# Optimization experiments

Measured on AMD Instinct MI355X. Metric: run time of the kernel, lower is better.

Reference implementation:

```python
import jax, jax.numpy as jnp
import numpy as np

DIM = 512
HEADS = 8


def setup_inputs() -> dict:
    key = jax.random.key(0)
    ks = jax.random.split(key, 9)
    s = 1.0 / np.sqrt(DIM)
    x = jax.random.normal(ks[0], (2, 4096, DIM), dtype=jnp.float32)
    Wq = jax.random.uniform(ks[1], (DIM, DIM), jnp.float32, -s, s)
    bq = jax.random.uniform(ks[2], (DIM,), jnp.float32, -s, s)
    Wk = jax.random.uniform(ks[3], (DIM, DIM), jnp.float32, -s, s)
    bk = jax.random.uniform(ks[4], (DIM,), jnp.float32, -s, s)
    Wv = jax.random.uniform(ks[5], (DIM, DIM), jnp.float32, -s, s)
    bv = jax.random.uniform(ks[6], (DIM,), jnp.float32, -s, s)
    Wo = jax.random.uniform(ks[7], (DIM, DIM), jnp.float32, -s, s)
    bo = jax.random.uniform(ks[8], (DIM,), jnp.float32, -s, s)
    return {"x": x, "Wq": Wq, "bq": bq, "Wk": Wk, "bk": bk,
            "Wv": Wv, "bv": bv, "Wo": Wo, "bo": bo}


def reference(x, Wq, bq, Wk, bk, Wv, bv, Wo, bo):
    b, t, d = x.shape
    h = HEADS
    dq = d // h
    scale = dq ** -0.5
    # projections: torch Linear is x @ W.T + b
    q = (x @ Wq.T + bq).reshape(b, t, h, dq)
    k = (x @ Wk.T + bk).reshape(b, t, h, dq)
    v = (x @ Wv.T + bv).reshape(b, t, h, dq)
    # attention scores [b, h, t, t] (full O(T^2) matrix, as in the original)
    att = jnp.einsum("bqhd,bkhd->bhqk", q, k) * scale
    att = jax.nn.softmax(att, axis=-1)
    out = jnp.einsum("bhqk,bkhd->bqhd", att, v).reshape(b, t, d)
    return out @ Wo.T + bo
```

## Files before the change

kernel.cpp:

```cpp
#include <hip/hip_runtime.h>

typedef short bf16x8 __attribute__((ext_vector_type(8)));
typedef float f32x4 __attribute__((ext_vector_type(4)));
typedef unsigned u32x2 __attribute__((ext_vector_type(2)));
typedef unsigned u32x4 __attribute__((ext_vector_type(4)));

#define MFMA(a, b, c) __builtin_amdgcn_mfma_f32_16x16x32_bf16((a), (b), (c), 0, 0, 0)

__device__ __forceinline__ unsigned cvtpk(float a, float b) {
    unsigned r;
    asm("v_cvt_pk_bf16_f32 %0, %1, %2" : "=v"(r) : "v"(a), "v"(b));
    return r;
}

__device__ __forceinline__ void gload16(const void* g, void* l) {
    __builtin_amdgcn_global_load_lds(
        (const __attribute__((address_space(1))) unsigned*)g,
        (__attribute__((address_space(3))) unsigned*)l, 16, 0, 0);
}

__global__ __launch_bounds__(256) void cvt_kernel(
    const float* __restrict__ x,
    const float* __restrict__ w0, const float* __restrict__ w1,
    const float* __restrict__ w2, const float* __restrict__ w3,
    unsigned short* __restrict__ xd,
    unsigned short* __restrict__ d0, unsigned short* __restrict__ d1,
    unsigned short* __restrict__ d2, unsigned short* __restrict__ d3)
{
    int bid = blockIdx.x;
    const float* src;
    unsigned short* dst;
    int off;
    if (bid < 4096) { src = x; dst = xd; off = bid; }
    else {
        int s = (bid - 4096) >> 8;
        src = s == 0 ? w0 : (s == 1 ? w1 : (s == 2 ? w2 : w3));
        dst = s == 0 ? d0 : (s == 1 ? d1 : (s == 2 ? d2 : d3));
        off = (bid - 4096) & 255;
    }
    size_t i = ((size_t)off * 256 + threadIdx.x) * 4;
    float4 v = *(const float4*)(src + i);
    uint2 pk;
    pk.x = cvtpk(v.x, v.y);
    pk.y = cvtpk(v.z, v.w);
    *(uint2*)(dst + i) = pk;
}

__device__ __forceinline__ void gemm128_core(
    const unsigned short* __restrict__ A, const unsigned short* __restrict__ W,
    int m0, int n0, int tid, unsigned short* sA, unsigned short* sB,
    f32x4 acc[4][4])
{
    const int lane = tid & 63, wid = tid >> 6;
    const int quad = lane >> 4, l15 = lane & 15;
    const int wm = wid >> 1, wn = wid & 1;

    const int gl_r = lane >> 3;
    const int gl_kc = (lane & 7) ^ gl_r;

    #pragma unroll
    for (int i = 0; i < 4; i++)
        #pragma unroll
        for (int j = 0; j < 4; j++) {
            f32x4 z = {0.f, 0.f, 0.f, 0.f};
            acc[i][j] = z;
        }

    for (int k0 = 0; k0 < 512; k0 += 64) {
        #pragma unroll
        for (int p = 0; p < 4; p++) {
            int chunk = wid * 4 + p;
            int row = chunk * 8 + gl_r;
            gload16(A + (size_t)(m0 + row) * 512 + k0 + gl_kc * 8,
                    (char*)sA + chunk * 1024);
            gload16(W + (size_t)(n0 + row) * 512 + k0 + gl_kc * 8,
                    (char*)sB + chunk * 1024);
        }
        __syncthreads();
        #pragma unroll
        for (int ks = 0; ks < 2; ks++) {
            bf16x8 af[4], bfr[4];
            #pragma unroll
            for (int i = 0; i < 4; i++) {
                int row = wm * 64 + i * 16 + l15;
                int kc = ks * 4 + quad;
                af[i] = *(const bf16x8*)((const char*)sA + row * 128 + ((kc ^ (row & 7)) << 4));
            }
            #pragma unroll
            for (int j = 0; j < 4; j++) {
                int row = wn * 64 + j * 16 + l15;
                int kc = ks * 4 + quad;
                bfr[j] = *(const bf16x8*)((const char*)sB + row * 128 + ((kc ^ (row & 7)) << 4));
            }
            #pragma unroll
            for (int i = 0; i < 4; i++)
                #pragma unroll
                for (int j = 0; j < 4; j++)
                    acc[i][j] = MFMA(af[i], bfr[j], acc[i][j]);
        }
        __syncthreads();
    }
}

__global__ __launch_bounds__(256) void qkv_kernel(
    const unsigned short* __restrict__ x,
    const unsigned short* __restrict__ Wq, const float* __restrict__ bq,
    const unsigned short* __restrict__ Wk, const float* __restrict__ bk,
    const unsigned short* __restrict__ Wv, const float* __restrict__ bv,
    unsigned short* __restrict__ qo, unsigned short* __restrict__ ko,
    unsigned short* __restrict__ vo)
{
    __shared__ unsigned short sA[128 * 64];
    __shared__ unsigned short sB[128 * 64];
    const int tid = threadIdx.x;
    const int by = blockIdx.y;
    const int sel = by >> 2;
    const int n0 = (by & 3) * 128;
    const int m0 = blockIdx.x * 128;
    const unsigned short* W = sel == 0 ? Wq : (sel == 1 ? Wk : Wv);
    const float* bias = sel == 0 ? bq : (sel == 1 ? bk : bv);

    f32x4 acc[4][4];
    gemm128_core(x, W, m0, n0, tid, sA, sB, acc);

    const int lane = tid & 63, wid = tid >> 6;
    const int quad = lane >> 4, l15 = lane & 15;
    const int wm = wid >> 1, wn = wid & 1;
    float bv4[4];
    #pragma unroll
    for (int j = 0; j < 4; j++) bv4[j] = bias[n0 + wn * 64 + j * 16 + l15];

    if (sel == 2) {
        #pragma unroll
        for (int i = 0; i < 4; i++) {
            #pragma unroll
            for (int j = 0; j < 4; j++) {
                int n = n0 + wn * 64 + j * 16 + l15;
                int h = n >> 6, d = n & 63;
                int m = m0 + wm * 64 + i * 16 + quad * 4;
                int b = m >> 12, t = m & 4095;
                uint2 pk;
                pk.x = cvtpk(acc[i][j][0] + bv4[j], acc[i][j][1] + bv4[j]);
                pk.y = cvtpk(acc[i][j][2] + bv4[j], acc[i][j][3] + bv4[j]);
                *(uint2*)(vo + ((size_t)(b * 8 + h) * 64 + d) * 4096 + t) = pk;
            }
        }
    } else {
        const float SC = (sel == 0) ? 0.125f * 1.44269504088896f : 1.0f;
        unsigned short* dst = sel == 0 ? qo : ko;
        #pragma unroll
        for (int i = 0; i < 4; i++) {
            #pragma unroll
            for (int j = 0; j < 4; j++) {
                int n = n0 + wn * 64 + j * 16 + l15;
                int h = n >> 6, d = n & 63;
                int m = m0 + wm * 64 + i * 16 + quad * 4;
                int b = m >> 12, t = m & 4095;
                size_t base2 = ((size_t)(b * 8 + h) * 4096 + t) * 64 + d;
                unsigned p01 = cvtpk((acc[i][j][0] + bv4[j]) * SC,
                                     (acc[i][j][1] + bv4[j]) * SC);
                unsigned p23 = cvtpk((acc[i][j][2] + bv4[j]) * SC,
                                     (acc[i][j][3] + bv4[j]) * SC);
                dst[base2]       = (unsigned short)p01;
                dst[base2 + 64]  = (unsigned short)(p01 >> 16);
                dst[base2 + 128] = (unsigned short)p23;
                dst[base2 + 192] = (unsigned short)(p23 >> 16);
            }
        }
    }
}

__global__ __launch_bounds__(512, 4) void attn_kernel(
    const unsigned short* __restrict__ qg, const unsigned short* __restrict__ kg,
    const unsigned short* __restrict__ vtg, unsigned short* __restrict__ og)
{
    __shared__ unsigned char smem[66048];

    const int tid = threadIdx.x;
    const int lane = tid & 63;
    const int w = tid >> 6;
    const int g = tid >> 8;
    const int wg = w & 3;
    const int sw = w & 3;
    const int quad = lane >> 4, l15 = lane & 15;
    const int bh = blockIdx.y;
    const size_t base = (size_t)bh * 4096 * 64;
    const unsigned short* Q = qg + base;
    const unsigned short* K = kg + base;
    const unsigned short* VT = vtg + base;
    const int qt0 = blockIdx.x * 128;

    const int srow = lane >> 3;
    const int skc  = (lane & 7) ^ srow;

    bf16x8 qf[2][2];
    #pragma unroll
    for (int cb = 0; cb < 2; cb++) {
        int q = qt0 + sw * 32 + cb * 16 + l15;
        #pragma unroll
        for (int ks = 0; ks < 2; ks++)
            qf[cb][ks] = *(const bf16x8*)(Q + (size_t)q * 64 + ks * 32 + quad * 8);
    }

    f32x4 ot[4][2];
    #pragma unroll
    for (int i = 0; i < 4; i++)
        #pragma unroll
        for (int cb = 0; cb < 2; cb++) {
            f32x4 z = {0.f, 0.f, 0.f, 0.f};
            ot[i][cb] = z;
        }
    f32x4 ls[2];
    {
        f32x4 z = {0.f, 0.f, 0.f, 0.f};
        ls[0] = z; ls[1] = z;
    }
    const short one_b = (short)0x3F80;
    const bf16x8 ones = {one_b, one_b, one_b, one_b, one_b, one_b, one_b, one_b};

    {
        int kb = g * 64;
        unsigned char* bK = smem + g * 8192;
        unsigned char* bV = smem + 16384 + g * 8192;
        #pragma unroll
        for (int p = 0; p < 2; p++) {
            int chunk = wg * 2 + p;
            int row = chunk * 8 + srow;
            gload16(K + (size_t)(kb + row) * 64 + skc * 8, bK + chunk * 1024);
            gload16(VT + (size_t)row * 4096 + kb + skc * 8, bV + chunk * 1024);
        }
    }

    int buf = 0;
    for (int it = 0; it < 32; it++) {
        __asm__ __volatile__("s_waitcnt vmcnt(0)" ::: "memory");
        __syncthreads();

        if (it < 31) {
            int kb = (2 * (it + 1) + g) * 64;
            unsigned char* bK = smem + (buf ^ 1) * 32768 + g * 8192;
            unsigned char* bV = smem + (buf ^ 1) * 32768 + 16384 + g * 8192;
            #pragma unroll
            for (int p = 0; p < 2; p++) {
                int chunk = wg * 2 + p;
                int row = chunk * 8 + srow;
                gload16(K + (size_t)(kb + row) * 64 + skc * 8, bK + chunk * 1024);
                gload16(VT + (size_t)row * 4096 + kb + skc * 8, bV + chunk * 1024);
            }
        }

        unsigned short* sK  = (unsigned short*)(smem + buf * 32768 + g * 8192);
        unsigned short* sVt = (unsigned short*)(smem + buf * 32768 + 16384 + g * 8192);

        #pragma unroll
        for (int half = 0; half < 2; half++) {
            unsigned xA[2], yA[2], zB[2], wB[2];
            #pragma unroll
            for (int rb2 = 0; rb2 < 2; rb2++) {
                int rb = half * 2 + rb2;
                int row = rb * 16 + l15;
                f32x4 s0 = {0.f, 0.f, 0.f, 0.f};
                f32x4 s1 = {0.f, 0.f, 0.f, 0.f};
                __builtin_amdgcn_s_setprio(1);
                #pragma unroll
                for (int ks = 0; ks < 2; ks++) {
                    int kc = ks * 4 + quad;
                    bf16x8 ka = *(const bf16x8*)((const char*)sK + row * 128 + ((kc ^ (row & 7)) << 4));
                    s0 = MFMA(ka, qf[0][ks], s0);
                    s1 = MFMA(ka, qf[1][ks], s1);
                }
                __builtin_amdgcn_s_setprio(0);
                unsigned e0 = cvtpk(__builtin_amdgcn_exp2f(s0[0]),
                                    __builtin_amdgcn_exp2f(s0[1]));
                unsigned e1 = cvtpk(__builtin_amdgcn_exp2f(s0[2]),
                                    __builtin_amdgcn_exp2f(s0[3]));
                unsigned f0 = cvtpk(__builtin_amdgcn_exp2f(s1[0]),
                                    __builtin_amdgcn_exp2f(s1[1]));
                unsigned f1 = cvtpk(__builtin_amdgcn_exp2f(s1[2]),
                                    __builtin_amdgcn_exp2f(s1[3]));
                if (rb2 == 0) { xA[0] = e0; yA[0] = e1; xA[1] = f0; yA[1] = f1; }
                else          { zB[0] = e0; wB[0] = e1; zB[1] = f0; wB[1] = f1; }
            }

            bf16x8 pf[2];
            #pragma unroll
            for (int cb = 0; cb < 2; cb++) {
                u32x2 s  = __builtin_amdgcn_permlane32_swap(xA[cb], zB[cb], false, false);
                u32x2 t  = __builtin_amdgcn_permlane16_swap(s[0], s[1], false, false);
                u32x2 s2 = __builtin_amdgcn_permlane32_swap(yA[cb], wB[cb], false, false);
                u32x2 t2 = __builtin_amdgcn_permlane16_swap(s2[0], s2[1], false, false);
                u32x4 fr = { t[0], t2[0], t[1], t2[1] };
                pf[cb] = __builtin_bit_cast(bf16x8, fr);
            }

            {
                int ks2 = half;
                __builtin_amdgcn_s_setprio(1);
                ls[0] = MFMA(ones, pf[0], ls[0]);
                ls[1] = MFMA(ones, pf[1], ls[1]);
                #pragma unroll
                for (int rbd = 0; rbd < 4; rbd++) {
                    int row = rbd * 16 + l15;
                    int kc = ks2 * 4 + quad;
                    bf16x8 vf = *(const bf16x8*)((const char*)sVt + row * 128 + ((kc ^ (row & 7)) << 4));
                    ot[rbd][0] = MFMA(vf, pf[0], ot[rbd][0]);
                    ot[rbd][1] = MFMA(vf, pf[1], ot[rbd][1]);
                }
                __builtin_amdgcn_s_setprio(0);
            }
        }
        buf ^= 1;
    }

    float* oc = (float*)smem;
    float* lc = (float*)(smem + 65536);
    if (g == 1) {
        #pragma unroll
        for (int cb = 0; cb < 2; cb++) {
            int qb = sw * 32 + cb * 16 + l15;
            if (quad == 0) lc[qb] = ls[cb][0];
            #pragma unroll
            for (int rbd = 0; rbd < 4; rbd++) {
                int dc = rbd * 4 + quad;
                *(f32x4*)((char*)oc + qb * 256 + ((dc ^ (qb & 15)) << 4)) = ot[rbd][cb];
            }
        }
    }
    __syncthreads();
    if (g == 0) {
        const int b = bh >> 3, h = bh & 7;
        #pragma unroll
        for (int cb = 0; cb < 2; cb++) {
            int qb = sw * 32 + cb * 16 + l15;
            float inv = 1.f / (ls[cb][0] + lc[qb]);
            int q = qt0 + qb;
            #pragma unroll
            for (int rbd = 0; rbd < 4; rbd++) {
                int dc = rbd * 4 + quad;
                f32x4 o2 = *(const f32x4*)((char*)oc + qb * 256 + ((dc ^ (qb & 15)) << 4));
                uint2 pk;
                pk.x = cvtpk((ot[rbd][cb][0] + o2[0]) * inv,
                             (ot[rbd][cb][1] + o2[1]) * inv);
                pk.y = cvtpk((ot[rbd][cb][2] + o2[2]) * inv,
                             (ot[rbd][cb][3] + o2[3]) * inv);
                *(uint2*)(og + ((size_t)(b * 4096 + q) * 512 + h * 64 + rbd * 16 + quad * 4)) = pk;
            }
        }
    }
}

__global__ __launch_bounds__(256) void out_kernel(
    const unsigned short* __restrict__ attn,
    const unsigned short* __restrict__ Wo, const float* __restrict__ bo,
    float* __restrict__ out)
{
    __shared__ unsigned short sA[128 * 64];
    __shared__ unsigned short sB[128 * 64];
    const int tid = threadIdx.x;
    const int m0 = blockIdx.x * 128;
    const int n0 = blockIdx.y * 128;

    f32x4 acc[4][4];
    gemm128_core(attn, Wo, m0, n0, tid, sA, sB, acc);

    const int lane = tid & 63, wid = tid >> 6;
    const int quad = lane >> 4, l15 = lane & 15;
    const int wm = wid >> 1, wn = wid & 1;
    float bv4[4];
    #pragma unroll
    for (int j = 0; j < 4; j++) bv4[j] = bo[n0 + wn * 64 + j * 16 + l15];
    #pragma unroll
    for (int i = 0; i < 4; i++) {
        #pragma unroll
        for (int j = 0; j < 4; j++) {
            int n = n0 + wn * 64 + j * 16 + l15;
            #pragma unroll
            for (int r = 0; r < 4; r++) {
                int m = m0 + wm * 64 + i * 16 + quad * 4 + r;
                out[(size_t)m * 512 + n] = acc[i][j][r] + bv4[j];
            }
        }
    }
}

extern "C" void kernel_launch(void* const* d_in, const int* in_sizes, int n_in,
                              void* d_out, int out_size, void* d_ws, size_t ws_size,
                              hipStream_t stream) {
    const float* x  = (const float*)d_in[0];
    const float* Wq = (const float*)d_in[1];
    const float* bq = (const float*)d_in[2];
    const float* Wk = (const float*)d_in[3];
    const float* bk = (const float*)d_in[4];
    const float* Wv = (const float*)d_in[5];
    const float* bv = (const float*)d_in[6];
    const float* Wo = (const float*)d_in[7];
    const float* bo = (const float*)d_in[8];
    unsigned short* ws = (unsigned short*)d_ws;

    const size_t NTOK = (size_t)2 * 4096 * 512;
    const size_t WSZ = (size_t)512 * 512;
    unsigned short* xb  = ws;
    unsigned short* Wqb = ws + NTOK;
    unsigned short* Wkb = Wqb + WSZ;
    unsigned short* Wvb = Wkb + WSZ;
    unsigned short* Wob = Wvb + WSZ;
    unsigned short* q_ws = Wob + WSZ;
    unsigned short* k_ws = q_ws + NTOK;
    unsigned short* v_ws = k_ws + NTOK;
    unsigned short* a_ws = v_ws + NTOK;

    cvt_kernel<<<5120, 256, 0, stream>>>(x, Wq, Wk, Wv, Wo, xb, Wqb, Wkb, Wvb, Wob);
    qkv_kernel<<<dim3(64, 12), 256, 0, stream>>>(xb, Wqb, bq, Wkb, bk, Wvb, bv,
                                                 q_ws, k_ws, v_ws);
    attn_kernel<<<dim3(32, 16), 512, 0, stream>>>(q_ws, k_ws, v_ws, a_ws);
    out_kernel<<<dim3(64, 4), 256, 0, stream>>>(a_ws, Wob, bo,
                                                (float*)d_out);
}
```

Measured before the change: 189.7 us.

## Store Q transposed with coalesced writes, precompute LDS offsets, unroll attention loop by two

Q is now written from the projection kernel in the transposed [d][t] layout with packed 8-byte stores, as V already was, replacing four scattered 2-byte stores per fragment. The attention kernel then gathers Q fragments with strided scalar loads, a one-time cost per block. It also precomputes the per-lane global and LDS swizzle offsets and unrolls the main loop by two so the double-buffer offset is a compile-time constant. The aim is cheaper projection stores and less address arithmetic in the hot loop, at the cost of more registers and slower Q loads.

```diff
diff --git a/kernel.cpp b/kernel.cpp
--- a/kernel.cpp
+++ b/kernel.cpp
@@ -130,7 +130,9 @@
     #pragma unroll
     for (int j = 0; j < 4; j++) bv4[j] = bias[n0 + wn * 64 + j * 16 + l15];
 
-    if (sel == 2) {
+    if (sel != 1) {
+        const float SC = (sel == 0) ? 0.125f * 1.44269504088896f : 1.0f;
+        unsigned short* dstT = (sel == 0) ? qo : vo;
         #pragma unroll
         for (int i = 0; i < 4; i++) {
             #pragma unroll
@@ -140,14 +142,14 @@
                 int m = m0 + wm * 64 + i * 16 + quad * 4;
                 int b = m >> 12, t = m & 4095;
                 uint2 pk;
-                pk.x = cvtpk(acc[i][j][0] + bv4[j], acc[i][j][1] + bv4[j]);
-                pk.y = cvtpk(acc[i][j][2] + bv4[j], acc[i][j][3] + bv4[j]);
-                *(uint2*)(vo + ((size_t)(b * 8 + h) * 64 + d) * 4096 + t) = pk;
+                pk.x = cvtpk((acc[i][j][0] + bv4[j]) * SC,
+                             (acc[i][j][1] + bv4[j]) * SC);
+                pk.y = cvtpk((acc[i][j][2] + bv4[j]) * SC,
+                             (acc[i][j][3] + bv4[j]) * SC);
+                *(uint2*)(dstT + ((size_t)(b * 8 + h) * 64 + d) * 4096 + t) = pk;
             }
         }
     } else {
-        const float SC = (sel == 0) ? 0.125f * 1.44269504088896f : 1.0f;
-        unsigned short* dst = sel == 0 ? qo : ko;
         #pragma unroll
         for (int i = 0; i < 4; i++) {
             #pragma unroll
@@ -157,14 +159,12 @@
                 int m = m0 + wm * 64 + i * 16 + quad * 4;
                 int b = m >> 12, t = m & 4095;
                 size_t base2 = ((size_t)(b * 8 + h) * 4096 + t) * 64 + d;
-                unsigned p01 = cvtpk((acc[i][j][0] + bv4[j]) * SC,
-                                     (acc[i][j][1] + bv4[j]) * SC);
-                unsigned p23 = cvtpk((acc[i][j][2] + bv4[j]) * SC,
-                                     (acc[i][j][3] + bv4[j]) * SC);
-                dst[base2]       = (unsigned short)p01;
-                dst[base2 + 64]  = (unsigned short)(p01 >> 16);
-                dst[base2 + 128] = (unsigned short)p23;
-                dst[base2 + 192] = (unsigned short)(p23 >> 16);
+                unsigned p01 = cvtpk(acc[i][j][0] + bv4[j], acc[i][j][1] + bv4[j]);
+                unsigned p23 = cvtpk(acc[i][j][2] + bv4[j], acc[i][j][3] + bv4[j]);
+                ko[base2]       = (unsigned short)p01;
+                ko[base2 + 64]  = (unsigned short)(p01 >> 16);
+                ko[base2 + 128] = (unsigned short)p23;
+                ko[base2 + 192] = (unsigned short)(p23 >> 16);
             }
         }
     }
@@ -193,13 +193,41 @@
     const int srow = lane >> 3;
     const int skc  = (lane & 7) ^ srow;
 
+    int kLaneOff[2], vLaneOff[2], dKOff[2], dVOff[2];
+    #pragma unroll
+    for (int p = 0; p < 2; p++) {
+        int chunk = wg * 2 + p;
+        int row = chunk * 8 + srow;
+        kLaneOff[p] = row * 64 + skc * 8;
+        vLaneOff[p] = row * 4096 + skc * 8;
+        dKOff[p] = g * 8192 + chunk * 1024;
+        dVOff[p] = 16384 + g * 8192 + chunk * 1024;
+    }
+
+    int okS[4][2], okV[4][2];
+    #pragma unroll
+    for (int rb = 0; rb < 4; rb++)
+        #pragma unroll
+        for (int ks = 0; ks < 2; ks++) {
+            int row = rb * 16 + l15;
+            int kc = ks * 4 + quad;
+            int sl = ((kc ^ (row & 7)) << 4);
+            okS[rb][ks] = g * 8192 + row * 128 + sl;
+            okV[rb][ks] = 16384 + g * 8192 + row * 128 + sl;
+        }
+
     bf16x8 qf[2][2];
     #pragma unroll
     for (int cb = 0; cb < 2; cb++) {
-        int q = qt0 + sw * 32 + cb * 16 + l15;
-        #pragma unroll
-        for (int ks = 0; ks < 2; ks++)
-            qf[cb][ks] = *(const bf16x8*)(Q + (size_t)q * 64 + ks * 32 + quad * 8);
+        int t = qt0 + sw * 32 + cb * 16 + l15;
+        #pragma unroll
+        for (int ks = 0; ks < 2; ks++) {
+            bf16x8 v;
+            #pragma unroll
+            for (int e = 0; e < 8; e++)
+                v[e] = (short)Q[(size_t)(ks * 32 + quad * 8 + e) * 4096 + t];
+            qf[cb][ks] = v;
+        }
     }
 
     f32x4 ot[4][2];
@@ -220,37 +248,26 @@
 
     {
         int kb = g * 64;
-        unsigned char* bK = smem + g * 8192;
-        unsigned char* bV = smem + 16384 + g * 8192;
         #pragma unroll
         for (int p = 0; p < 2; p++) {
-            int chunk = wg * 2 + p;
-            int row = chunk * 8 + srow;
-            gload16(K + (size_t)(kb + row) * 64 + skc * 8, bK + chunk * 1024);
-            gload16(VT + (size_t)row * 4096 + kb + skc * 8, bV + chunk * 1024);
-        }
-    }
-
-    int buf = 0;
-    for (int it = 0; it < 32; it++) {
+            gload16(K + (size_t)kb * 64 + kLaneOff[p], smem + dKOff[p]);
+            gload16(VT + (size_t)kb + vLaneOff[p], smem + dVOff[p]);
+        }
+    }
+
+    auto do_iter = [&](int it, int bufoff) {
         __asm__ __volatile__("s_waitcnt vmcnt(0)" ::: "memory");
         __syncthreads();
 
         if (it < 31) {
             int kb = (2 * (it + 1) + g) * 64;
-            unsigned char* bK = smem + (buf ^ 1) * 32768 + g * 8192;
-            unsigned char* bV = smem + (buf ^ 1) * 32768 + 16384 + g * 8192;
+            int od = bufoff ^ 32768;
             #pragma unroll
             for (int p = 0; p < 2; p++) {
-                int chunk = wg * 2 + p;
-                int row = chunk * 8 + srow;
-                gload16(K + (size_t)(kb + row) * 64 + skc * 8, bK + chunk * 1024);
-                gload16(VT + (size_t)row * 4096 + kb + skc * 8, bV + chunk * 1024);
-            }
-        }
-
-        unsigned short* sK  = (unsigned short*)(smem + buf * 32768 + g * 8192);
-        unsigned short* sVt = (unsigned short*)(smem + buf * 32768 + 16384 + g * 8192);
+                gload16(K + (size_t)kb * 64 + kLaneOff[p], smem + od + dKOff[p]);
+                gload16(VT + (size_t)kb + vLaneOff[p], smem + od + dVOff[p]);
+            }
+        }
 
         #pragma unroll
         for (int half = 0; half < 2; half++) {
@@ -258,14 +275,12 @@
             #pragma unroll
             for (int rb2 = 0; rb2 < 2; rb2++) {
                 int rb = half * 2 + rb2;
-                int row = rb * 16 + l15;
                 f32x4 s0 = {0.f, 0.f, 0.f, 0.f};
                 f32x4 s1 = {0.f, 0.f, 0.f, 0.f};
                 __builtin_amdgcn_s_setprio(1);
                 #pragma unroll
                 for (int ks = 0; ks < 2; ks++) {
-                    int kc = ks * 4 + quad;
-                    bf16x8 ka = *(const bf16x8*)((const char*)sK + row * 128 + ((kc ^ (row & 7)) << 4));
+                    bf16x8 ka = *(const bf16x8*)(smem + bufoff + okS[rb][ks]);
                     s0 = MFMA(ka, qf[0][ks], s0);
                     s1 = MFMA(ka, qf[1][ks], s1);
                 }
@@ -293,23 +308,22 @@
                 pf[cb] = __builtin_bit_cast(bf16x8, fr);
             }
 
-            {
-                int ks2 = half;
-                __builtin_amdgcn_s_setprio(1);
-                ls[0] = MFMA(ones, pf[0], ls[0]);
-                ls[1] = MFMA(ones, pf[1], ls[1]);
-                #pragma unroll
-                for (int rbd = 0; rbd < 4; rbd++) {
-                    int row = rbd * 16 + l15;
-                    int kc = ks2 * 4 + quad;
-                    bf16x8 vf = *(const bf16x8*)((const char*)sVt + row * 128 + ((kc ^ (row & 7)) << 4));
-                    ot[rbd][0] = MFMA(vf, pf[0], ot[rbd][0]);
-                    ot[rbd][1] = MFMA(vf, pf[1], ot[rbd][1]);
-                }
-                __builtin_amdgcn_s_setprio(0);
-            }
-        }
-        buf ^= 1;
+            __builtin_amdgcn_s_setprio(1);
+            ls[0] = MFMA(ones, pf[0], ls[0]);
+            ls[1] = MFMA(ones, pf[1], ls[1]);
+            #pragma unroll
+            for (int rbd = 0; rbd < 4; rbd++) {
+                bf16x8 vf = *(const bf16x8*)(smem + bufoff + okV[rbd][half]);
+                ot[rbd][0] = MFMA(vf, pf[0], ot[rbd][0]);
+                ot[rbd][1] = MFMA(vf, pf[1], ot[rbd][1]);
+            }
+            __builtin_amdgcn_s_setprio(0);
+        }
+    };
+
+    for (int it2 = 0; it2 < 16; it2++) {
+        do_iter(2 * it2, 0);
+        do_iter(2 * it2 + 1, 32768);
     }
 
     float* oc = (float*)smem;
```

New measurement: 190.5 us. No clear change (+0.4%).
